# Performance work log

Hardware: AMD Instinct MI355X
Metric: run time of the kernel (lower is better)

## Reference

```python
import jax, jax.numpy as jnp
import numpy as np

EMBED_DIM = 768
NUM_HEADS = 12
HEAD_DIM = EMBED_DIM // NUM_HEADS
SEQ_LEN = 196
NUM_CLASSES = 3
BATCH = 256


def setup_inputs() -> dict:
    key = jax.random.key(0)
    ks = jax.random.split(key, 7)
    s = 0.02
    return {
        "x": jax.random.normal(ks[0], (BATCH, SEQ_LEN * EMBED_DIM), dtype=jnp.float32),
        "qkv_w": jax.random.normal(ks[1], (EMBED_DIM, 3 * EMBED_DIM), dtype=jnp.float32) * s,
        "qkv_b": jax.random.normal(ks[2], (3 * EMBED_DIM,), dtype=jnp.float32) * s,
        "out_w": jax.random.normal(ks[3], (EMBED_DIM, EMBED_DIM), dtype=jnp.float32) * s,
        "out_b": jax.random.normal(ks[4], (EMBED_DIM,), dtype=jnp.float32) * s,
        "cls_w": jax.random.normal(ks[5], (SEQ_LEN * EMBED_DIM, NUM_CLASSES), dtype=jnp.float32) * s,
        "cls_b": jax.random.normal(ks[6], (NUM_CLASSES,), dtype=jnp.float32) * s,
    }


def reference(x, qkv_w, qkv_b, out_w, out_b, cls_w, cls_b):
    B = x.shape[0]
    # (B, S*E) -> (B, S, E)
    xt = x.reshape(B, SEQ_LEN, EMBED_DIM)
    # QKV projection: (B, S, 3E) -> (B, S, H, 3*hd)
    qkv = (xt @ qkv_w + qkv_b).reshape(B, SEQ_LEN, NUM_HEADS, 3 * HEAD_DIM)
    q, k, v = jnp.split(qkv, 3, axis=-1)  # each (B, S, H, hd)
    # NOTE: faithful to source — attention is over the HEADS axis (HxH per token),
    # because q @ k.transpose(-2,-1) acts on the last two dims of (B,S,H,hd).
    scale = 1.0 / (HEAD_DIM ** 0.5)
    scores = jnp.einsum("bsid,bsjd->bsij", q, k) * scale  # (B, S, H, H)
    attn = jax.nn.softmax(scores, axis=-1)
    out = jnp.einsum("bsij,bsjd->bsid", attn, v).reshape(B, SEQ_LEN, EMBED_DIM)
    out = out @ out_w + out_b                 # (B, S, E)
    out = out.reshape(B, SEQ_LEN * EMBED_DIM)  # flatten(1)
    return out @ cls_w + cls_b                # (B, num_classes)
```

## Files before the change

kernel.cpp:

```cpp
#include <hip/hip_runtime.h>

typedef _Float16 f16;
typedef _Float16 f16x8 __attribute__((ext_vector_type(8)));
typedef float f32x4 __attribute__((ext_vector_type(4)));

#define SEQ   196
#define EMB   768
#define NHEAD 12
#define HD    64
#define BATCH 256
#define TOK   (BATCH*SEQ)
#define QKVN  (3*EMB)
#define CLSK  (SEQ*EMB)

#define GLD16(gp, lp) __builtin_amdgcn_global_load_lds( \
    (const __attribute__((address_space(1))) void*)(gp), \
    (__attribute__((address_space(3))) void*)(lp), 16, 0, 0)

__global__ __launch_bounds__(256) void k_cvt8(const float* __restrict__ in,
                                              f16* __restrict__ out, int n8) {
  int i = blockIdx.x * 256 + threadIdx.x;
  if (i >= n8) return;
  const float4* p = (const float4*)in + (size_t)i * 2;
  float4 a = p[0], b = p[1];
  f16x8 o;
  o[0]=(f16)a.x; o[1]=(f16)a.y; o[2]=(f16)a.z; o[3]=(f16)a.w;
  o[4]=(f16)b.x; o[5]=(f16)b.y; o[6]=(f16)b.z; o[7]=(f16)b.w;
  *((f16x8*)out + i) = o;
}

__global__ __launch_bounds__(256) void k_transpose_cvt(const float* __restrict__ W,
                                                       f16* __restrict__ WT,
                                                       int K, int N) {
  __shared__ float tile[32][33];
  int n0 = blockIdx.x * 32, k0 = blockIdx.y * 32;
  int t = threadIdx.x, tx = t & 31, ty = t >> 5;
  #pragma unroll
  for (int i = 0; i < 4; ++i) {
    int r = ty + i * 8;
    tile[r][tx] = W[(size_t)(k0 + r) * N + n0 + tx];
  }
  __syncthreads();
  #pragma unroll
  for (int i = 0; i < 4; ++i) {
    int r = ty + i * 8;
    WT[(size_t)(n0 + r) * K + k0 + tx] = (f16)tile[tx][r];
  }
}

__global__ __launch_bounds__(256) void k_extract_cls(const float* __restrict__ cls_w,
                                                     f16* __restrict__ cls16,
                                                     float* __restrict__ zbias) {
  int idx = blockIdx.x * 256 + threadIdx.x;
  int r = idx / EMB, e = idx - r * EMB;
  int c = r / SEQ, s = r - c * SEQ;
  cls16[(size_t)r * EMB + e] = (f16)cls_w[((size_t)s * EMB + e) * 3 + c];
  if (blockIdx.x == 0)
    for (int i = threadIdx.x; i < EMB; i += 256) zbias[i] = 0.f;
}

__global__ __launch_bounds__(256) void k_const3a(const float* __restrict__ out_b,
                                                 const float* __restrict__ cls_w,
                                                 float* __restrict__ partial) {
  int s = blockIdx.x, t = threadIdx.x;
  float a0 = 0.f, a1 = 0.f, a2 = 0.f;
  for (int e = t; e < EMB; e += 256) {
    float ob = out_b[e];
    const float* p = cls_w + ((size_t)s * EMB + e) * 3;
    a0 += ob * p[0]; a1 += ob * p[1]; a2 += ob * p[2];
  }
  __shared__ float r0[256], r1[256], r2[256];
  r0[t] = a0; r1[t] = a1; r2[t] = a2;
  __syncthreads();
  for (int off = 128; off > 0; off >>= 1) {
    if (t < off) { r0[t] += r0[t + off]; r1[t] += r1[t + off]; r2[t] += r2[t + off]; }
    __syncthreads();
  }
  if (t == 0) { partial[s * 3 + 0] = r0[0]; partial[s * 3 + 1] = r1[0]; partial[s * 3 + 2] = r2[0]; }
}

__global__ __launch_bounds__(64) void k_const3b(const float* __restrict__ partial,
                                                const float* __restrict__ cls_b,
                                                float* __restrict__ const3) {
  int t = threadIdx.x;
  #pragma unroll
  for (int c = 0; c < 3; ++c) {
    float s = 0.f;
    for (int j = t; j < SEQ; j += 64) s += partial[j * 3 + c];
    #pragma unroll
    for (int off = 32; off > 0; off >>= 1) s += __shfl_down(s, off, 64);
    if (t == 0) const3[c] = s + cls_b[c];
  }
}

__global__ __launch_bounds__(256) void k_make_w2p(const f16* __restrict__ W2c,
                                                  float* __restrict__ W2p) {
  int idx = blockIdx.x * 256 + threadIdx.x;
  int r = idx / EMB, e = idx - r * EMB;
  int c = r / SEQ, s = r - c * SEQ;
  W2p[((size_t)s * EMB + e) * 4 + c] = (float)W2c[idx];
}

__global__ __launch_bounds__(256) void k_gemm_bias(
    const f16* __restrict__ A, const f16* __restrict__ Bm,
    const float* __restrict__ bias, f16* __restrict__ C,
    int M, int N, int K) {
  __shared__ f16 As[128 * 64];
  __shared__ f16 Bs[128 * 64];
  const int t = threadIdx.x;
  const int l = t & 63;
  const int w = t >> 6;
  const int wr = w >> 1, wc = w & 1;

  const int nwg = gridDim.x;
  const int orig = blockIdx.x;
  const int q = nwg >> 3, r8 = nwg & 7;
  const int xcd = orig & 7, seq = orig >> 3;
  const int base = xcd < r8 ? xcd * (q + 1) : r8 * (q + 1) + (xcd - r8) * q;
  const int wg = base + seq;
  const int NB = N >> 7;
  const int bm = wg / NB, bn = wg - bm * NB;

  const size_t rowA0 = (size_t)bm * 128, rowB0 = (size_t)bn * 128;
  f32x4 acc[4][4] = {};

  for (int k0 = 0; k0 < K; k0 += 64) {
    if (k0) __syncthreads();
    #pragma unroll
    for (int i = 0; i < 4; ++i) {
      int qq = i * 256 + t;
      int rr = qq >> 3, c = qq & 7;
      int cs = c ^ (rr & 7);
      const f16* ga = A  + (rowA0 + rr) * K + k0 + cs * 8;
      const f16* gb = Bm + (rowB0 + rr) * K + k0 + cs * 8;
      f16* la = As + (size_t)(i * 256 + w * 64) * 8;
      f16* lb = Bs + (size_t)(i * 256 + w * 64) * 8;
      GLD16(ga, la);
      GLD16(gb, lb);
    }
    __syncthreads();
    #pragma unroll
    for (int ks = 0; ks < 2; ++ks) {
      f16x8 av[4], bv[4];
      const int k8 = ks * 4 + (l >> 4);
      #pragma unroll
      for (int m = 0; m < 4; ++m) {
        int rr = wr * 64 + m * 16 + (l & 15);
        av[m] = *(const f16x8*)((const char*)As + rr * 128 + ((k8 ^ (rr & 7)) << 4));
      }
      #pragma unroll
      for (int n = 0; n < 4; ++n) {
        int rr = wc * 64 + n * 16 + (l & 15);
        bv[n] = *(const f16x8*)((const char*)Bs + rr * 128 + ((k8 ^ (rr & 7)) << 4));
      }
      #pragma unroll
      for (int m = 0; m < 4; ++m)
        #pragma unroll
        for (int n = 0; n < 4; ++n)
          acc[m][n] = __builtin_amdgcn_mfma_f32_16x16x32_f16(av[m], bv[n], acc[m][n], 0, 0, 0);
    }
  }
  #pragma unroll
  for (int n = 0; n < 4; ++n) {
    int gcol = bn * 128 + wc * 64 + n * 16 + (l & 15);
    float bs = bias[gcol];
    #pragma unroll
    for (int m = 0; m < 4; ++m) {
      int grow0 = bm * 128 + wr * 64 + m * 16 + (l >> 4) * 4;
      #pragma unroll
      for (int j = 0; j < 4; ++j)
        C[(size_t)(grow0 + j) * N + gcol] = (f16)(acc[m][n][j] + bs);
    }
  }
}

__global__ __launch_bounds__(64) void k_attn_cls(const f16* __restrict__ qkv,
                                                 const float* __restrict__ W2p,
                                                 float* __restrict__ part4) {
  const int s = blockIdx.x, b = blockIdx.y;
  const int tok = b * SEQ + s;
  const int l = threadIdx.x;
  __shared__ f16 row[QKVN];
  __shared__ float sc[144];
  __shared__ float aw[144];
  const uint2* src = (const uint2*)(qkv + (size_t)tok * QKVN);
  uint2* dst = (uint2*)row;
  #pragma unroll
  for (int i = 0; i < 9; ++i) dst[l + i * 64] = src[l + i * 64];
  __syncthreads();
  for (int p = l; p < 144; p += 64) {
    int i = p / 12, j = p - i * 12;
    const f16x8* q8 = (const f16x8*)(row + i * 192);
    const f16x8* k8 = (const f16x8*)(row + j * 192 + 64);
    float sv = 0.f;
    #pragma unroll
    for (int d8 = 0; d8 < 8; ++d8) {
      f16x8 a = q8[d8], bb = k8[d8];
      #pragma unroll
      for (int e = 0; e < 8; ++e) sv += (float)a[e] * (float)bb[e];
    }
    sc[p] = sv * 0.125f;
  }
  __syncthreads();
  if (l < 12) {
    float m = -1e30f;
    #pragma unroll
    for (int j = 0; j < 12; ++j) m = fmaxf(m, sc[l * 12 + j]);
    float e[12], sum = 0.f;
    #pragma unroll
    for (int j = 0; j < 12; ++j) { e[j] = __expf(sc[l * 12 + j] - m); sum += e[j]; }
    float inv = 1.f / sum;
    #pragma unroll
    for (int j = 0; j < 12; ++j) aw[l * 12 + j] = e[j] * inv;
  }
  __syncthreads();
  float vv[12];
  #pragma unroll
  for (int j = 0; j < 12; ++j) vv[j] = (float)row[j * 192 + 128 + l];
  const float4* wrow = (const float4*)W2p + (size_t)s * EMB;
  float s0 = 0.f, s1 = 0.f, s2 = 0.f;
  #pragma unroll
  for (int i = 0; i < 12; ++i) {
    float o = 0.f;
    #pragma unroll
    for (int j = 0; j < 12; ++j) o += aw[i * 12 + j] * vv[j];
    float4 wv = wrow[i * 64 + l];
    s0 += o * wv.x; s1 += o * wv.y; s2 += o * wv.z;
  }
  #pragma unroll
  for (int off = 32; off > 0; off >>= 1) {
    s0 += __shfl_down(s0, off, 64);
    s1 += __shfl_down(s1, off, 64);
    s2 += __shfl_down(s2, off, 64);
  }
  if (l == 0) *(float4*)(part4 + (size_t)tok * 4) = make_float4(s0, s1, s2, 0.f);
}

__global__ __launch_bounds__(64) void k_cls_final(const float* __restrict__ part4,
                                                  const float* __restrict__ const3,
                                                  float* __restrict__ logits) {
  const int b = blockIdx.x, l = threadIdx.x;
  float s0 = 0.f, s1 = 0.f, s2 = 0.f;
  for (int j = l; j < SEQ; j += 64) {
    float4 p = *(const float4*)(part4 + ((size_t)b * SEQ + j) * 4);
    s0 += p.x; s1 += p.y; s2 += p.z;
  }
  #pragma unroll
  for (int off = 32; off > 0; off >>= 1) {
    s0 += __shfl_down(s0, off, 64);
    s1 += __shfl_down(s1, off, 64);
    s2 += __shfl_down(s2, off, 64);
  }
  if (l == 0) {
    logits[b * 3 + 0] = s0 + const3[0];
    logits[b * 3 + 1] = s1 + const3[1];
    logits[b * 3 + 2] = s2 + const3[2];
  }
}

extern "C" void kernel_launch(void* const* d_in, const int* in_sizes, int n_in,
                              void* d_out, int out_size, void* d_ws, size_t ws_size,
                              hipStream_t stream) {
  (void)in_sizes; (void)n_in; (void)out_size;
  const float* x      = (const float*)d_in[0];
  const float* qkv_w  = (const float*)d_in[1];
  const float* qkv_b  = (const float*)d_in[2];
  const float* out_w  = (const float*)d_in[3];
  const float* out_b  = (const float*)d_in[4];
  const float* cls_w  = (const float*)d_in[5];
  const float* cls_b  = (const float*)d_in[6];
  float* logits = (float*)d_out;

  const size_t SZ_X16 = (size_t)TOK * EMB * 2;
  const size_t SZ_QKV = (size_t)TOK * QKVN * 2;
  const size_t SZ_QT  = (size_t)QKVN * EMB * 2;
  const size_t SZ_OT  = (size_t)EMB * EMB * 2;
  if (ws_size < SZ_X16 + SZ_QKV + SZ_QT + SZ_OT) return;

  char* ws = (char*)d_ws;
  const size_t base2 = SZ_X16 + SZ_QKV;
  f16*   x16     = (f16*)ws;
  float* W2p     = (float*)(ws);
  f16*   outw16  = (f16*)(ws + (4u << 20));
  f16*   cls16   = (f16*)(ws + (8u << 20));
  f16*   W2c     = (f16*)(ws + (12u << 20));
  float* partial = (float*)(ws + (16u << 20));
  float* part4   = (float*)(ws + (20u << 20));
  float* zbias   = (float*)(ws + (24u << 20));
  float* const3  = (float*)(ws + (25u << 20));
  f16*   qkvb    = (f16*)(ws + SZ_X16);
  f16*   qkvT    = (f16*)(ws + base2);

  k_cvt8<<<dim3(TOK * EMB / 8 / 256), dim3(256), 0, stream>>>(x, x16, TOK * EMB / 8);
  k_transpose_cvt<<<dim3(QKVN / 32, EMB / 32), dim3(256), 0, stream>>>(qkv_w, qkvT, EMB, QKVN);
  k_gemm_bias<<<dim3((TOK / 128) * (QKVN / 128)), dim3(256), 0, stream>>>(x16, qkvT, qkv_b, qkvb, TOK, QKVN, EMB);
  k_cvt8<<<dim3(EMB * EMB / 8 / 256), dim3(256), 0, stream>>>(out_w, outw16, EMB * EMB / 8);
  k_extract_cls<<<dim3(588 * EMB / 256), dim3(256), 0, stream>>>(cls_w, cls16, zbias);
  k_const3a<<<dim3(SEQ), dim3(256), 0, stream>>>(out_b, cls_w, partial);
  k_const3b<<<dim3(1), dim3(64), 0, stream>>>(partial, cls_b, const3);
  k_gemm_bias<<<dim3((640 / 128) * (EMB / 128)), dim3(256), 0, stream>>>(cls16, outw16, zbias, W2c, 640, EMB, EMB);
  k_make_w2p<<<dim3(588 * EMB / 256), dim3(256), 0, stream>>>(W2c, W2p);
  k_attn_cls<<<dim3(SEQ, BATCH), dim3(64), 0, stream>>>(qkvb, W2p, part4);
  k_cls_final<<<dim3(BATCH), dim3(64), 0, stream>>>(part4, const3, logits);
}
```

Before: 374.5 us.

## Replace QKV GEMM with 256x256 tiled, ping-pong pipelined MFMA kernel

Adds a new 512-thread GEMM kernel with 256x256 output tiles, double-buffered swizzled LDS loads via global_load_lds, an 8-phase schedule that interleaves LDS reads, async global loads and MFMA blocks under barriers with s_setprio, and XCD-aware workgroup remapping. The QKV projection now uses it instead of the 128x128 kernel. The goal is more operand reuse per tile and better overlap of memory traffic with matrix math in the dominant GEMM. The cost is high register pressure from 32 accumulators per thread, and exact divisibility is assumed: TOK=50176 is 196*256, so it divides.

```diff
diff --git a/kernel.cpp b/kernel.cpp
--- a/kernel.cpp
+++ b/kernel.cpp
@@ -170,6 +170,214 @@
       #pragma unroll
       for (int j = 0; j < 4; ++j)
         C[(size_t)(grow0 + j) * N + gcol] = (f16)(acc[m][n][j] + bs);
+    }
+  }
+}
+
+__global__ __launch_bounds__(512, 2) void k_gemm256(
+    const f16* __restrict__ A, const f16* __restrict__ Bm,
+    const float* __restrict__ bias, f16* __restrict__ C,
+    int M, int N, int K) {
+  __shared__ f16 As[2 * 256 * 64];
+  __shared__ f16 Bs[2 * 256 * 64];
+  const int t = threadIdx.x;
+  const int l = t & 63;
+  const int w = t >> 6;
+  const int wm = w >> 2;
+  const int wn = w & 3;
+
+  const int nwg = gridDim.x;
+  const int orig = blockIdx.x;
+  const int q = nwg >> 3, r8 = nwg & 7;
+  const int xcd = orig & 7, seq = orig >> 3;
+  const int base = xcd < r8 ? xcd * (q + 1) : r8 * (q + 1) + (xcd - r8) * q;
+  const int wg = base + seq;
+  const int NB = N >> 8;
+  const int bm = wg / NB, bn = wg - bm * NB;
+
+  const size_t rowA0 = (size_t)bm * 256, rowB0 = (size_t)bn * 256;
+  const int KT = K >> 6;
+
+  f32x4 acc[8][4] = {};
+  f16x8 a[4][2], b0[2][2], b1[2][2];
+
+  auto stageA = [&](int kt, int rd) {
+    if (kt >= KT) return;
+    int qq = rd * 512 + t;
+    int rr = qq >> 3, c = qq & 7;
+    int cs = c ^ (rr & 7);
+    GLD16(A + (rowA0 + rr) * (size_t)K + kt * 64 + cs * 8,
+          As + (kt & 1) * 16384 + qq * 8);
+  };
+  auto stageB = [&](int kt, int rd) {
+    if (kt >= KT) return;
+    int qq = rd * 512 + t;
+    int rr = qq >> 3, c = qq & 7;
+    int cs = c ^ (rr & 7);
+    GLD16(Bm + (rowB0 + rr) * (size_t)K + kt * 64 + cs * 8,
+          Bs + (kt & 1) * 16384 + qq * 8);
+  };
+  auto rdA = [&](int buf, int mi, int kk) -> f16x8 {
+    int rr = wm * 128 + mi * 16 + (l & 15);
+    int k8 = kk * 4 + (l >> 4);
+    return *(const f16x8*)((const char*)As + buf * 32768 + rr * 128 + ((k8 ^ (rr & 7)) << 4));
+  };
+  auto rdB = [&](int buf, int ni, int kk) -> f16x8 {
+    int rr = wn * 64 + ni * 16 + (l & 15);
+    int k8 = kk * 4 + (l >> 4);
+    return *(const f16x8*)((const char*)Bs + buf * 32768 + rr * 128 + ((k8 ^ (rr & 7)) << 4));
+  };
+  auto drain = [&](int kt) {
+    if (kt < KT) { asm volatile("s_waitcnt vmcnt(8)" ::: "memory"); }
+    else         { asm volatile("s_waitcnt vmcnt(0)" ::: "memory"); }
+  };
+
+#define PH_SYNC_PRE()  asm volatile("" ::: "memory"); __builtin_amdgcn_s_barrier(); \
+                       __builtin_amdgcn_s_setprio(1)
+#define PH_SYNC_POST() __builtin_amdgcn_s_setprio(0); asm volatile("" ::: "memory"); \
+                       __builtin_amdgcn_s_barrier()
+
+  #pragma unroll
+  for (int rd = 0; rd < 4; ++rd) { stageA(0, rd); stageB(0, rd); }
+  #pragma unroll
+  for (int rd = 0; rd < 4; ++rd) { stageA(1, rd); stageB(1, rd); }
+  asm volatile("s_waitcnt vmcnt(8)" ::: "memory");
+  __builtin_amdgcn_s_barrier();
+
+  for (int it = 0; it < KT / 2; ++it) {
+    const int t2 = 2 * it + 2, t3 = 2 * it + 3;
+
+    #pragma unroll
+    for (int i = 0; i < 4; ++i)
+      #pragma unroll
+      for (int kk = 0; kk < 2; ++kk) a[i][kk] = rdA(0, i, kk);
+    #pragma unroll
+    for (int ni = 0; ni < 2; ++ni)
+      #pragma unroll
+      for (int kk = 0; kk < 2; ++kk) b0[ni][kk] = rdB(0, ni, kk);
+    PH_SYNC_PRE();
+    #pragma unroll
+    for (int i = 0; i < 4; ++i)
+      #pragma unroll
+      for (int ni = 0; ni < 2; ++ni)
+        #pragma unroll
+        for (int kk = 0; kk < 2; ++kk)
+          acc[i][ni] = __builtin_amdgcn_mfma_f32_16x16x32_f16(a[i][kk], b0[ni][kk], acc[i][ni], 0, 0, 0);
+    PH_SYNC_POST();
+
+    #pragma unroll
+    for (int ni = 0; ni < 2; ++ni)
+      #pragma unroll
+      for (int kk = 0; kk < 2; ++kk) b1[ni][kk] = rdB(0, 2 + ni, kk);
+    stageA(t2, 0); stageA(t2, 2);
+    PH_SYNC_PRE();
+    #pragma unroll
+    for (int i = 0; i < 4; ++i)
+      #pragma unroll
+      for (int ni = 0; ni < 2; ++ni)
+        #pragma unroll
+        for (int kk = 0; kk < 2; ++kk)
+          acc[i][2 + ni] = __builtin_amdgcn_mfma_f32_16x16x32_f16(a[i][kk], b1[ni][kk], acc[i][2 + ni], 0, 0, 0);
+    PH_SYNC_POST();
+
+    #pragma unroll
+    for (int i = 0; i < 4; ++i)
+      #pragma unroll
+      for (int kk = 0; kk < 2; ++kk) a[i][kk] = rdA(0, 4 + i, kk);
+    stageB(t2, 0); stageB(t2, 1); stageB(t2, 2); stageB(t2, 3);
+    PH_SYNC_PRE();
+    #pragma unroll
+    for (int i = 0; i < 4; ++i)
+      #pragma unroll
+      for (int ni = 0; ni < 2; ++ni)
+        #pragma unroll
+        for (int kk = 0; kk < 2; ++kk)
+          acc[4 + i][2 + ni] = __builtin_amdgcn_mfma_f32_16x16x32_f16(a[i][kk], b1[ni][kk], acc[4 + i][2 + ni], 0, 0, 0);
+    PH_SYNC_POST();
+
+    stageA(t2, 1); stageA(t2, 3);
+    drain(t2);
+    PH_SYNC_PRE();
+    #pragma unroll
+    for (int i = 0; i < 4; ++i)
+      #pragma unroll
+      for (int ni = 0; ni < 2; ++ni)
+        #pragma unroll
+        for (int kk = 0; kk < 2; ++kk)
+          acc[4 + i][ni] = __builtin_amdgcn_mfma_f32_16x16x32_f16(a[i][kk], b0[ni][kk], acc[4 + i][ni], 0, 0, 0);
+    PH_SYNC_POST();
+
+    #pragma unroll
+    for (int i = 0; i < 4; ++i)
+      #pragma unroll
+      for (int kk = 0; kk < 2; ++kk) a[i][kk] = rdA(1, i, kk);
+    #pragma unroll
+    for (int ni = 0; ni < 2; ++ni)
+      #pragma unroll
+      for (int kk = 0; kk < 2; ++kk) b0[ni][kk] = rdB(1, ni, kk);
+    PH_SYNC_PRE();
+    #pragma unroll
+    for (int i = 0; i < 4; ++i)
+      #pragma unroll
+      for (int ni = 0; ni < 2; ++ni)
+        #pragma unroll
+        for (int kk = 0; kk < 2; ++kk)
+          acc[i][ni] = __builtin_amdgcn_mfma_f32_16x16x32_f16(a[i][kk], b0[ni][kk], acc[i][ni], 0, 0, 0);
+    PH_SYNC_POST();
+
+    #pragma unroll
+    for (int ni = 0; ni < 2; ++ni)
+      #pragma unroll
+      for (int kk = 0; kk < 2; ++kk) b1[ni][kk] = rdB(1, 2 + ni, kk);
+    stageA(t3, 0); stageA(t3, 2);
+    PH_SYNC_PRE();
+    #pragma unroll
+    for (int i = 0; i < 4; ++i)
+      #pragma unroll
+      for (int ni = 0; ni < 2; ++ni)
+        #pragma unroll
+        for (int kk = 0; kk < 2; ++kk)
+          acc[i][2 + ni] = __builtin_amdgcn_mfma_f32_16x16x32_f16(a[i][kk], b1[ni][kk], acc[i][2 + ni], 0, 0, 0);
+    PH_SYNC_POST();
+
+    #pragma unroll
+    for (int i = 0; i < 4; ++i)
+      #pragma unroll
+      for (int kk = 0; kk < 2; ++kk) a[i][kk] = rdA(1, 4 + i, kk);
+    stageB(t3, 0); stageB(t3, 1); stageB(t3, 2); stageB(t3, 3);
+    PH_SYNC_PRE();
+    #pragma unroll
+    for (int i = 0; i < 4; ++i)
+      #pragma unroll
+      for (int ni = 0; ni < 2; ++ni)
+        #pragma unroll
+        for (int kk = 0; kk < 2; ++kk)
+          acc[4 + i][2 + ni] = __builtin_amdgcn_mfma_f32_16x16x32_f16(a[i][kk], b1[ni][kk], acc[4 + i][2 + ni], 0, 0, 0);
+    PH_SYNC_POST();
+
+    stageA(t3, 1); stageA(t3, 3);
+    drain(t3);
+    PH_SYNC_PRE();
+    #pragma unroll
+    for (int i = 0; i < 4; ++i)
+      #pragma unroll
+      for (int ni = 0; ni < 2; ++ni)
+        #pragma unroll
+        for (int kk = 0; kk < 2; ++kk)
+          acc[4 + i][ni] = __builtin_amdgcn_mfma_f32_16x16x32_f16(a[i][kk], b0[ni][kk], acc[4 + i][ni], 0, 0, 0);
+    PH_SYNC_POST();
+  }
+
+  #pragma unroll
+  for (int ni = 0; ni < 4; ++ni) {
+    int gcol = bn * 256 + wn * 64 + ni * 16 + (l & 15);
+    float bs = bias[gcol];
+    #pragma unroll
+    for (int mi = 0; mi < 8; ++mi) {
+      int grow0 = bm * 256 + wm * 128 + mi * 16 + (l >> 4) * 4;
+      #pragma unroll
+      for (int j = 0; j < 4; ++j)
+        C[(size_t)(grow0 + j) * N + gcol] = (f16)(acc[mi][ni][j] + bs);
     }
   }
 }
@@ -293,7 +501,7 @@
 
   k_cvt8<<<dim3(TOK * EMB / 8 / 256), dim3(256), 0, stream>>>(x, x16, TOK * EMB / 8);
   k_transpose_cvt<<<dim3(QKVN / 32, EMB / 32), dim3(256), 0, stream>>>(qkv_w, qkvT, EMB, QKVN);
-  k_gemm_bias<<<dim3((TOK / 128) * (QKVN / 128)), dim3(256), 0, stream>>>(x16, qkvT, qkv_b, qkvb, TOK, QKVN, EMB);
+  k_gemm256<<<dim3((TOK / 256) * (QKVN / 256)), dim3(512), 0, stream>>>(x16, qkvT, qkv_b, qkvb, TOK, QKVN, EMB);
   k_cvt8<<<dim3(EMB * EMB / 8 / 256), dim3(256), 0, stream>>>(out_w, outw16, EMB * EMB / 8);
   k_extract_cls<<<dim3(588 * EMB / 256), dim3(256), 0, stream>>>(cls_w, cls16, zbias);
   k_const3a<<<dim3(SEQ), dim3(256), 0, stream>>>(out_b, cls_w, partial);
```

Result: no change. 378.0 us (+0.9%).
